# Performance work log

Measured on AMD Instinct MI355X. Metric: run time of the kernel, lower is better.

Reference implementation:

```python
import jax, jax.numpy as jnp
import numpy as np

CONF_T = 0.6   # default conf_threshold
IOU_T = 0.5    # default iou_threshold
ALPHA = 0.25
GAMMA = 2.0


def _nms_np(boxes, scores, iou_t):
    """Greedy NMS (torchvision semantics: keep while IoU <= iou_t), returns kept indices
    into `boxes`, sorted by decreasing score. Pure numpy; data-dependent output size."""
    order = np.argsort(-scores, kind="stable")
    b = boxes[order]
    x1, y1, x2, y2 = b[:, 0], b[:, 1], b[:, 2], b[:, 3]
    areas = (x2 - x1) * (y2 - y1)
    M = b.shape[0]
    suppressed = np.zeros(M, dtype=bool)
    keep = []
    for i in range(M):
        if suppressed[i]:
            continue
        keep.append(order[i])
        if i + 1 >= M:
            break
        xx1 = np.maximum(x1[i], x1[i + 1:]); yy1 = np.maximum(y1[i], y1[i + 1:])
        xx2 = np.minimum(x2[i], x2[i + 1:]); yy2 = np.minimum(y2[i], y2[i + 1:])
        inter = np.clip(xx2 - xx1, 0, None) * np.clip(yy2 - yy1, 0, None)
        iou = inter / (areas[i] + areas[i + 1:] - inter)
        suppressed[i + 1:] |= iou > iou_t
    return np.asarray(keep, dtype=np.int64)


def _select_indices(loc, conf):
    """Concrete (non-traced) confidence filtering + NMS; index selection is
    non-differentiable in the original torch code as well."""
    conf_np = np.asarray(conf)
    if conf_np.ndim == 3:
        conf_np = conf_np[0]                      # conf.squeeze(0)
    scores = conf_np.max(axis=1)                  # conf.max(dim=1)
    filt_idx = np.nonzero(scores > CONF_T)[0]     # mask filter
    boxes = np.asarray(loc)[0, filt_idx]          # loc[:, mask, :].squeeze(0)
    nms_score = conf_np[filt_idx, 0]              # score = filtered_conf[:, 0]
    nms_keep = _nms_np(boxes, nms_score, IOU_T)
    return filt_idx, nms_keep


def _smooth_l1_sum(pred, target):
    # SmoothL1Loss(beta=1.0, reduction='sum'); target (k,4) broadcasts against
    # pred (k,C,4) exactly as torch does (requires C == k).
    d = jnp.abs(pred - target)
    return jnp.sum(jnp.where(d < 1.0, 0.5 * d * d, d - 0.5))


def _loss(loc, conf, target_boxes, target_labels_f, filt_idx, nms_keep, k):
    conf2 = conf[0] if conf.ndim == 3 else conf   # (N,C)
    floc = loc[0, filt_idx]                       # (M,4) filtered boxes
    fconf = conf2[filt_idx]                       # (M,C)
    mloc = floc[nms_keep]                         # (P,4) NMS-kept boxes
    mconf = fconf[nms_keep]                       # (P,C)
    # torch.topk(matched_conf, k, dim=0): per-class column top-k
    vals, idx = jax.lax.top_k(mconf.T, k)         # (C,k) each
    vals, idx = vals.T, idx.T                     # (k,C)
    conf_bin = (vals[:, 0] > 0.5).astype(jnp.float32)   # (k,) hard 0/1 "logits"
    pred_box = mloc[idx]                          # (k,C,4) gather, as matched_loc[indices,:]
    loc_loss = _smooth_l1_sum(pred_box, target_boxes)
    # F.cross_entropy with 1-D input and float target => soft-label CE (scalar)
    ce = -jnp.sum(target_labels_f * jax.nn.log_softmax(conf_bin))
    p_t = jnp.exp(-ce)
    conf_loss = ALPHA * (1.0 - p_t) ** GAMMA * ce
    num_pos = jnp.asarray(nms_keep.shape[0], dtype=jnp.float32)
    return (loc_loss + conf_loss) / num_pos


def setup_inputs() -> dict:
    key = jax.random.key(0)
    k0, k1, k2, k3 = jax.random.split(key, 4)
    N, C, K = 8192, 20, 20
    return {
        "loc": jax.random.uniform(k0, (1, N, 4), dtype=jnp.float32),
        "conf": jax.random.uniform(k1, (1, N, C), dtype=jnp.float32),
        "target_boxes": jax.random.uniform(k2, (K, 4), dtype=jnp.float32),
        "target_labels": jax.random.randint(k3, (K,), 0, C).astype(jnp.int64),
    }


def reference(loc, conf, target_boxes, target_labels):
    filt_idx, nms_keep = _select_indices(loc, conf)
    if filt_idx.size == 0 or nms_keep.size == 0:
        return jnp.float32(0.001)
    k = int(target_labels.shape[0])
    return _loss(loc, conf, target_boxes,
                 target_labels.astype(jnp.float32),
                 jnp.asarray(filt_idx), jnp.asarray(nms_keep), k)
```

## Files before the change

kernel.cpp:

```cpp
#include <hip/hip_runtime.h>
#include <stdint.h>
#include <stddef.h>


#define NCAP 8192
#define WROW (NCAP / 64)

typedef unsigned long long u64;

constexpr size_t OFF_CNT   = 0;
constexpr size_t OFF_KEYS  = 256;
constexpr size_t OFF_SX1   = OFF_KEYS + 8ull * NCAP;
constexpr size_t OFF_SY1   = OFF_SX1 + 4ull * NCAP;
constexpr size_t OFF_SX2   = OFF_SY1 + 4ull * NCAP;
constexpr size_t OFF_SY2   = OFF_SX2 + 4ull * NCAP;
constexpr size_t OFF_AREA  = OFF_SY2 + 4ull * NCAP;
constexpr size_t OFF_SORIG = OFF_AREA + 4ull * NCAP;
constexpr size_t OFF_KEEPS = OFF_SORIG + 4ull * NCAP;
constexpr size_t OFF_KORIG = OFF_KEEPS + 4ull * NCAP;
constexpr size_t OFF_TOPV  = OFF_KORIG + 4ull * NCAP;
constexpr size_t OFF_TOPI  = OFF_TOPV + 4096;
constexpr size_t OFF_DIAG2 = OFF_TOPI + 4096;
constexpr size_t OFF_MASK  = OFF_DIAG2 + 16ull * NCAP;
constexpr size_t WS_NEED_MASK = OFF_MASK + 8ull * NCAP * WROW;

__device__ __forceinline__ void barrier_nodrain() {
  asm volatile("s_waitcnt lgkmcnt(0)" ::: "memory");
  __builtin_amdgcn_s_barrier();
  asm volatile("" ::: "memory");
}

template <int CTRL, int RMASK>
__device__ __forceinline__ unsigned or_dpp_step(unsigned x) {
  return x | (unsigned)__builtin_amdgcn_update_dpp(0, (int)x, CTRL, RMASK, 0xf, true);
}
__device__ __forceinline__ u64 wave_or64(u64 x) {
  unsigned lo = (unsigned)x, hi = (unsigned)(x >> 32);
  lo = or_dpp_step<0x111, 0xf>(lo); hi = or_dpp_step<0x111, 0xf>(hi);
  lo = or_dpp_step<0x112, 0xf>(lo); hi = or_dpp_step<0x112, 0xf>(hi);
  lo = or_dpp_step<0x114, 0xf>(lo); hi = or_dpp_step<0x114, 0xf>(hi);
  lo = or_dpp_step<0x118, 0xf>(lo); hi = or_dpp_step<0x118, 0xf>(hi);
  lo = or_dpp_step<0x142, 0xa>(lo); hi = or_dpp_step<0x142, 0xa>(hi);
  lo = or_dpp_step<0x143, 0xc>(lo); hi = or_dpp_step<0x143, 0xc>(hi);
  lo = (unsigned)__builtin_amdgcn_readlane((int)lo, 63);
  hi = (unsigned)__builtin_amdgcn_readlane((int)hi, 63);
  return ((u64)hi << 32) | lo;
}

#define SS1(M)                                                              \
  { int tt = base + (M) * 64 + l;                                           \
    u64 a = e[M];                                                           \
    unsigned slo = __shfl_xor((unsigned)a, (int)jj);                        \
    unsigned shi = __shfl_xor((unsigned)(a >> 32), (int)jj);                \
    u64 b = ((u64)shi << 32) | slo;                                         \
    bool up = ((tt & bk) == 0);                                             \
    bool lowr = ((l & (int)jj) == 0);                                       \
    bool tmin = (up == lowr);                                               \
    bool agtb = (a > b);                                                    \
    e[M] = (tmin == agtb) ? b : a; }

#define SSTEP() { SS1(0) SS1(1) SS1(2) SS1(3) SS1(4) SS1(5) SS1(6) SS1(7) }

#define CSW(A, B)                                                           \
  { int tt = base + (A) * 64 + l;                                           \
    bool up = ((tt & bk) == 0);                                             \
    u64 xa = e[A], xb = e[B];                                               \
    bool sw = up ? (xa > xb) : (xa < xb);                                   \
    e[A] = sw ? xb : xa; e[B] = sw ? xa : xb; }

#define RSTEP4() { CSW(0,4) CSW(1,5) CSW(2,6) CSW(3,7) }
#define RSTEP2() { CSW(0,2) CSW(1,3) CSW(4,6) CSW(5,7) }
#define RSTEP1() { CSW(0,1) CSW(2,3) CSW(4,5) CSW(6,7) }

__global__ __launch_bounds__(64) void k_psort(
    const float* __restrict__ conf, int N, int C,
    u64* __restrict__ keys) {
  const int l = threadIdx.x;
  const int base = blockIdx.x * 512;
  u64 e[8];
#pragma unroll
  for (int m = 0; m < 8; ++m) {
    int row = base + m * 64 + l;
    u64 key;
    if (row < N) {
      const float* cr = conf + (size_t)row * C;
      float mx = cr[0];
      for (int c = 1; c < C; ++c) mx = fmaxf(mx, cr[c]);
      unsigned int k32;
      if (mx > 0.6f) {
        union { float f; unsigned int u; } s; s.f = cr[0];
        unsigned int u = s.u;
        u = (u & 0x80000000u) ? ~u : (u | 0x80000000u);
        k32 = ~u;
        if (k32 == 0xFFFFFFFFu) k32 = 0xFFFFFFFEu;
      } else {
        k32 = 0xFFFFFFFFu;
      }
      key = ((u64)k32 << 32) | (unsigned int)row;
    } else {
      key = ((u64)0xFFFFFFFFu << 32);
    }
    e[m] = key;
  }
  for (unsigned bk = 2; bk <= 512; bk <<= 1) {
    unsigned j = bk >> 1;
    if (j == 256) { RSTEP4(); j = 128; }
    if (j == 128) { RSTEP2(); j = 64; }
    if (j == 64)  { RSTEP1(); j = 32; }
    for (unsigned jj = j; jj >= 1; jj >>= 1) SSTEP();
  }
#pragma unroll
  for (int m = 0; m < 8; ++m) keys[base + m * 64 + l] = e[m];
}

__global__ __launch_bounds__(1024) void k_merge(
    const float* __restrict__ loc,
    u64* __restrict__ keys, unsigned int* __restrict__ cnt,
    float* __restrict__ sx1, float* __restrict__ sy1,
    float* __restrict__ sx2, float* __restrict__ sy2,
    float* __restrict__ sarea, unsigned int* __restrict__ sorig) {
  __shared__ u64 sk[NCAP];
  __shared__ int wsum[16];
  const int tid = threadIdx.x;
  const int w = tid >> 6, l = tid & 63;
  const int base = w * 512;
  u64 e[8];
#pragma unroll
  for (int m = 0; m < 8; ++m) e[m] = keys[base + m * 64 + l];

  for (unsigned bk = 1024; bk <= NCAP; bk <<= 1) {
    unsigned j = bk >> 1;
    {
#pragma unroll
      for (int m = 0; m < 8; ++m) sk[base + m * 64 + l] = e[m];
      __syncthreads();
      for (unsigned j2 = bk >> 1; j2 >= 512; j2 >>= 1) {
        for (int tl = tid; tl < NCAP; tl += 1024) {
          unsigned p = (unsigned)tl ^ j2;
          if (p > (unsigned)tl) {
            bool up = ((tl & bk) == 0);
            u64 x = sk[tl], y = sk[p];
            bool sw = up ? (x > y) : (x < y);
            if (sw) { sk[tl] = y; sk[p] = x; }
          }
        }
        __syncthreads();
      }
#pragma unroll
      for (int m = 0; m < 8; ++m) e[m] = sk[base + m * 64 + l];
      __syncthreads();
      j = 256;
    }
    if (j == 256) { RSTEP4(); j = 128; }
    if (j == 128) { RSTEP2(); j = 64; }
    if (j == 64)  { RSTEP1(); j = 32; }
    for (unsigned jj = j; jj >= 1; jj >>= 1) SSTEP();
  }

  int cv = 0;
#pragma unroll
  for (int m = 0; m < 8; ++m) {
    int idx = base + m * 64 + l;
    u64 key = e[m];
    if ((key >> 32) != 0xFFFFFFFFull) ++cv;
    unsigned row = (unsigned)(key & 0xFFFFFFFFull);
    const float* b = loc + (size_t)row * 4;
    float x1 = b[0], y1 = b[1], x2 = b[2], y2 = b[3];
    sx1[idx] = x1; sy1[idx] = y1; sx2[idx] = x2; sy2[idx] = y2;
    sarea[idx] = (x2 - x1) * (y2 - y1);
    sorig[idx] = row;
  }
  for (int off = 32; off; off >>= 1) cv += __shfl_down(cv, off);
  if (l == 0) wsum[w] = cv;
  __syncthreads();
  if (tid == 0) {
    int s = 0;
    for (int i = 0; i < 16; ++i) s += wsum[i];
    cnt[0] = (unsigned int)s;
  }
}

__global__ __launch_bounds__(64) void k_mask(
    const float* __restrict__ sx1, const float* __restrict__ sy1,
    const float* __restrict__ sx2, const float* __restrict__ sy2,
    const float* __restrict__ sarea,
    u64* __restrict__ mask, u64* __restrict__ diagI) {
  if (blockIdx.y < (blockIdx.x & ~1u)) return;
  __shared__ float jx1[64], jy1[64], jx2[64], jy2[64], ja[64];
  int t = threadIdx.x;
  int jbase = blockIdx.y * 64;
  jx1[t] = sx1[jbase + t]; jy1[t] = sy1[jbase + t];
  jx2[t] = sx2[jbase + t]; jy2[t] = sy2[jbase + t];
  ja[t]  = sarea[jbase + t];
  __syncthreads();
  int i = blockIdx.x * 64 + t;
  float xi1 = sx1[i], yi1 = sy1[i], xi2 = sx2[i], yi2 = sy2[i], ai = sarea[i];
  u64 bits = 0ULL;
#pragma unroll 8
  for (int jj = 0; jj < 64; ++jj) {
    float xx1 = fmaxf(xi1, jx1[jj]);
    float yy1 = fmaxf(yi1, jy1[jj]);
    float xx2 = fminf(xi2, jx2[jj]);
    float yy2 = fminf(yi2, jy2[jj]);
    float w = fmaxf(xx2 - xx1, 0.0f);
    float h = fmaxf(yy2 - yy1, 0.0f);
    float inter = w * h;
    float den = ai + ja[jj] - inter;
    float iou = inter / den;
    if (iou > 0.5f) bits |= (1ULL << jj);
  }
  mask[(size_t)i * WROW + blockIdx.y] = bits;
  if ((blockIdx.y >> 1) == (blockIdx.x >> 1))
    diagI[((size_t)i << 1) + (blockIdx.y & 1)] = bits;
}

__global__ __launch_bounds__(1024) void k_scan(
    const u64* __restrict__ mask,
    const u64* __restrict__ diagIg,
    unsigned int* __restrict__ cnt,
    unsigned int* __restrict__ keeps) {
  __shared__ __align__(16) u64 ldsDiag[2 * NCAP];
  __shared__ __align__(16) u64 rem[WROW];
  __shared__ u64 ldsKA, ldsKB;
  __shared__ int ldsKb;
  const int tid = threadIdx.x;
  const int F = (int)cnt[0];
  const int nch = (F + 127) >> 7;
  const ulonglong2* __restrict__ m2 = (const ulonglong2*)mask;

  for (int i = tid; i < 2 * NCAP; i += 1024) ldsDiag[i] = diagIg[i];
  for (int w = tid; w < WROW; w += 1024) rem[w] = 0;

  const int p0 = tid & 63;
  const int g0 = tid >> 6;
  int K = 0;
  __syncthreads();

  for (int H = 0; H < nch; ++H) {
    const size_t gb = (size_t)H * 8192;
    const int base = H << 7;
    const bool ld = (p0 > H);
    ulonglong2 v0 = {0,0}, v1 = {0,0}, v2 = {0,0}, v3 = {0,0},
               v4 = {0,0}, v5 = {0,0}, v6 = {0,0}, v7 = {0,0};
    if (ld) {
      v0 = m2[gb + tid];
      v1 = m2[gb + tid + 1024];
      v2 = m2[gb + tid + 2048];
      v3 = m2[gb + tid + 3072];
      v4 = m2[gb + tid + 4096];
      v5 = m2[gb + tid + 5120];
      v6 = m2[gb + tid + 6144];
      v7 = m2[gb + tid + 7168];
    }
    barrier_nodrain();

    if (tid < 64) {
      ulonglong2 dAB = *(const ulonglong2*)&ldsDiag[(size_t)(base + tid) << 1];
      u64 DA = dAB.x, AB = dAB.y;
      u64 DB = ldsDiag[(((size_t)(base + 64 + tid)) << 1) + 1];
      ulonglong2 supP = *(const ulonglong2*)&rem[2 * H];
      u64 sup0 = supP.x, supB0 = supP.y;

      int remrows = F - base;
      u64 validA = (remrows >= 64) ? ~0ull : ((1ull << remrows) - 1ull);
      int r2 = remrows - 64;
      u64 validB = (r2 >= 64) ? ~0ull : ((r2 <= 0) ? 0ull : ((1ull << r2) - 1ull));

      u64 DfwdA = (tid < 63) ? (DA & (~0ull << (tid + 1))) : 0ull;
      u64 undec = validA & ~sup0;
      u64 dmask = ((undec >> tid) & 1ull) ? DfwdA : 0ull;
      u64 vuln = wave_or64(dmask);
      u64 dang = __ballot(dmask != 0ull);
      u64 involved = (dang | vuln) & undec;
      u64 keepA = undec & ~involved;
      u64 und2 = involved;
      {
        unsigned Flo = (unsigned)DfwdA, Fhi = (unsigned)(DfwdA >> 32);
        while (und2) {
          int rr = __builtin_ctzll(und2);
          keepA |= 1ull << rr;
          unsigned dlo = __builtin_amdgcn_readlane(Flo, rr);
          unsigned dhi = __builtin_amdgcn_readlane(Fhi, rr);
          und2 &= ~((((u64)dhi << 32) | (u64)dlo) | (1ull << rr));
        }
      }

      u64 abm = ((keepA >> tid) & 1ull) ? AB : 0ull;
      u64 supB = supB0 | wave_or64(abm);
      u64 DfwdB = (tid < 63) ? (DB & (~0ull << (tid + 1))) : 0ull;
      u64 undecB = validB & ~supB;
      u64 dmaskB = ((undecB >> tid) & 1ull) ? DfwdB : 0ull;
      u64 vulnB = wave_or64(dmaskB);
      u64 dangB = __ballot(dmaskB != 0ull);
      u64 involvedB = (dangB | vulnB) & undecB;
      u64 keepB = undecB & ~involvedB;
      u64 und2B = involvedB;
      {
        unsigned Flo = (unsigned)DfwdB, Fhi = (unsigned)(DfwdB >> 32);
        while (und2B) {
          int rr = __builtin_ctzll(und2B);
          keepB |= 1ull << rr;
          unsigned dlo = __builtin_amdgcn_readlane(Flo, rr);
          unsigned dhi = __builtin_amdgcn_readlane(Fhi, rr);
          und2B &= ~((((u64)dhi << 32) | (u64)dlo) | (1ull << rr));
        }
      }

      if (tid == 0) { ldsKA = keepA; ldsKB = keepB; ldsKb = K; }
      K += __popcll(keepA) + __popcll(keepB);
    }
    barrier_nodrain();

    const u64 keepA = ldsKA, keepB = ldsKB;

    if (g0 == 1) {
      const int l = p0;
      const int Kb = ldsKb;
      int pcA = __popcll(keepA);
      unsigned kloA = (unsigned)keepA, khiA = (unsigned)(keepA >> 32);
      int preA = __builtin_amdgcn_mbcnt_hi(khiA, __builtin_amdgcn_mbcnt_lo(kloA, 0));
      if ((keepA >> l) & 1ull) keeps[Kb + preA] = (unsigned)(base + l);
      unsigned kloB = (unsigned)keepB, khiB = (unsigned)(keepB >> 32);
      int preB = __builtin_amdgcn_mbcnt_hi(khiB, __builtin_amdgcn_mbcnt_lo(kloB, 0));
      if ((keepB >> l) & 1ull) keeps[Kb + pcA + preB] = (unsigned)(base + 64 + l);
    }

    if (ld && (keepA | keepB)) {
      u64 ax = 0, ay = 0;
      if ((keepA >> g0) & 1ull)        { ax |= v0.x; ay |= v0.y; }
      if ((keepA >> (g0+16)) & 1ull)   { ax |= v1.x; ay |= v1.y; }
      if ((keepA >> (g0+32)) & 1ull)   { ax |= v2.x; ay |= v2.y; }
      if ((keepA >> (g0+48)) & 1ull)   { ax |= v3.x; ay |= v3.y; }
      if ((keepB >> g0) & 1ull)        { ax |= v4.x; ay |= v4.y; }
      if ((keepB >> (g0+16)) & 1ull)   { ax |= v5.x; ay |= v5.y; }
      if ((keepB >> (g0+32)) & 1ull)   { ax |= v6.x; ay |= v6.y; }
      if ((keepB >> (g0+48)) & 1ull)   { ax |= v7.x; ay |= v7.y; }
      const int w0 = 2 * p0;
      if (ax) atomicOr(&rem[w0], ax);
      if (ay) atomicOr(&rem[w0 + 1], ay);
    }
  }
  if (tid == 0) cnt[1] = (unsigned int)K;
}

__global__ __launch_bounds__(256) void k_scan_nomask(
    const float* __restrict__ sx1, const float* __restrict__ sy1,
    const float* __restrict__ sx2, const float* __restrict__ sy2,
    const float* __restrict__ sarea,
    unsigned int* __restrict__ cnt,
    unsigned int* __restrict__ keeps) {
  __shared__ unsigned char sup[NCAP];
  __shared__ int sK;
  int tid = threadIdx.x;
  int F = (int)cnt[0];
  for (int j = tid; j < NCAP; j += 256) sup[j] = 0;
  if (tid == 0) sK = 0;
  __syncthreads();
  for (int i = 0; i < F; ++i) {
    if (!sup[i]) {
      if (tid == 0) keeps[sK++] = (unsigned int)i;
      float xi1 = sx1[i], yi1 = sy1[i], xi2 = sx2[i], yi2 = sy2[i], ai = sarea[i];
      for (int j = i + 1 + tid; j < F; j += 256) {
        if (sup[j]) continue;
        float xx1 = fmaxf(xi1, sx1[j]);
        float yy1 = fmaxf(yi1, sy1[j]);
        float xx2 = fminf(xi2, sx2[j]);
        float yy2 = fminf(yi2, sy2[j]);
        float w = fmaxf(xx2 - xx1, 0.0f);
        float h = fmaxf(yy2 - yy1, 0.0f);
        float inter = w * h;
        float iou = inter / (ai + sarea[j] - inter);
        if (iou > 0.5f) sup[j] = 1;
      }
    }
    __syncthreads();
  }
  if (tid == 0) cnt[1] = (unsigned int)sK;
}

__global__ __launch_bounds__(1024) void k_topk(
    const float* __restrict__ conf,
    const unsigned int* __restrict__ sorig,
    const unsigned int* __restrict__ keeps,
    const unsigned int* __restrict__ cnt,
    int C, int KT,
    float* __restrict__ topv, int* __restrict__ topi) {
  __shared__ float wlv[16];
  __shared__ int wli[16];
  __shared__ float ldsWv;
  __shared__ int ldsWj;
  const int tid = threadIdx.x;
  const int lane = tid & 63;
  const int wv_ = tid >> 6;
  const int c = blockIdx.x;
  const int M = (int)cnt[1];

  const float NEG = -3.402823466e+38f;
  float v[8];
#pragma unroll
  for (int k = 0; k < 8; ++k) {
    int j = tid + (k << 10);
    v[k] = (j < M) ? conf[(size_t)sorig[keeps[j]] * C + c] : NEG;
  }
  float bv = NEG; int bk_ = -1;
#pragma unroll
  for (int k = 0; k < 8; ++k)
    if (v[k] > bv) { bv = v[k]; bk_ = k; }
  int bj = (bk_ >= 0) ? (tid + (bk_ << 10)) : 0x7FFFFFFF;
  if (bv == NEG) bj = 0x7FFFFFFF;

  for (int t = 0; t < KT; ++t) {
    float rv = bv; int rj = bj;
#pragma unroll
    for (int off = 32; off; off >>= 1) {
      float v2 = __shfl_down(rv, off);
      int   j2 = __shfl_down(rj, off);
      if (v2 > rv || (v2 == rv && j2 < rj)) { rv = v2; rj = j2; }
    }
    if (lane == 0) { wlv[wv_] = rv; wli[wv_] = rj; }
    __syncthreads();
    if (wv_ == 0) {
      float fv = (lane < 16) ? wlv[lane] : NEG;
      int   fj = (lane < 16) ? wli[lane] : 0x7FFFFFFF;
#pragma unroll
      for (int off = 32; off; off >>= 1) {
        float v2 = __shfl_down(fv, off);
        int   j2 = __shfl_down(fj, off);
        if (v2 > fv || (v2 == fv && j2 < fj)) { fv = v2; fj = j2; }
      }
      if (lane == 0) {
        ldsWv = fv; ldsWj = fj;
        topv[c * KT + t] = fv;
        topi[c * KT + t] = (fj == 0x7FFFFFFF) ? 0 : fj;
      }
    }
    __syncthreads();
    const int wj = ldsWj;
    if (wj != 0x7FFFFFFF && (wj & 1023) == tid) {
      int kk = wj >> 10;
#pragma unroll
      for (int k = 0; k < 8; ++k)
        if (k == kk) v[k] = NEG;
      bv = NEG; bk_ = -1;
#pragma unroll
      for (int k = 0; k < 8; ++k)
        if (v[k] > bv) { bv = v[k]; bk_ = k; }
      bj = (bk_ >= 0) ? (tid + (bk_ << 10)) : 0x7FFFFFFF;
      if (bv == NEG) bj = 0x7FFFFFFF;
    }
  }
}

__global__ __launch_bounds__(256) void k_loss(
    const float* __restrict__ loc, const float* __restrict__ tb,
    const int* __restrict__ labels,
    const unsigned int* __restrict__ sorig,
    const unsigned int* __restrict__ keeps,
    const float* __restrict__ topv, const int* __restrict__ topi,
    const unsigned int* __restrict__ cnt, int C, int KT,
    float* __restrict__ out) {
  __shared__ float red[256];
  int tid = threadIdx.x;
  int F = (int)cnt[0];
  int M = (int)cnt[1];
  if (F == 0 || M == 0) {
    if (tid == 0) out[0] = 0.001f;
    return;
  }
  int total = KT * C * 4;
  float part = 0.0f;
  for (int e = tid; e < total; e += 256) {
    int d = e & 3;
    int q = e >> 2;
    int c = q % C;
    int i = q / C;
    int j = topi[c * KT + i];
    unsigned int orow = sorig[keeps[j]];
    float pred = loc[(size_t)orow * 4 + d];
    float tg = tb[c * 4 + d];
    float dd = fabsf(pred - tg);
    part += (dd < 1.0f) ? (0.5f * dd * dd) : (dd - 0.5f);
  }
  red[tid] = part;
  __syncthreads();
  for (int s = 128; s > 0; s >>= 1) {
    if (tid < s) red[tid] += red[tid + s];
    __syncthreads();
  }
  if (tid == 0) {
    float loc_loss = red[0];
    float mx = -3.402823466e+38f;
    for (int i = 0; i < KT; ++i) {
      float x = (topv[i] > 0.5f) ? 1.0f : 0.0f;
      mx = fmaxf(mx, x);
    }
    float ssum = 0.0f;
    for (int i = 0; i < KT; ++i) {
      float x = (topv[i] > 0.5f) ? 1.0f : 0.0f;
      ssum += expf(x - mx);
    }
    float lse = mx + logf(ssum);
    float ce = 0.0f;
    for (int i = 0; i < KT; ++i) {
      float x = (topv[i] > 0.5f) ? 1.0f : 0.0f;
      ce += (float)labels[i] * (x - lse);
    }
    ce = -ce;
    float pt = expf(-ce);
    float om = 1.0f - pt;
    float conf_loss = 0.25f * om * om * ce;
    out[0] = (loc_loss + conf_loss) / (float)M;
  }
}


extern "C" void kernel_launch(void* const* d_in, const int* in_sizes, int n_in,
                              void* d_out, int out_size, void* d_ws, size_t ws_size,
                              hipStream_t stream) {
  (void)n_in; (void)out_size;
  const float* loc    = (const float*)d_in[0];
  const float* conf   = (const float*)d_in[1];
  const float* tb     = (const float*)d_in[2];
  const int*   labels = (const int*)d_in[3];
  float* out = (float*)d_out;

  int N = in_sizes[0] / 4;
  if (N > NCAP) N = NCAP;
  int C  = (N > 0) ? (in_sizes[1] / N) : 20;
  int KT = in_sizes[3];

  char* ws = (char*)d_ws;
  unsigned int* cnt   = (unsigned int*)(ws + OFF_CNT);
  u64*          keys  = (u64*)(ws + OFF_KEYS);
  float*        sx1   = (float*)(ws + OFF_SX1);
  float*        sy1   = (float*)(ws + OFF_SY1);
  float*        sx2   = (float*)(ws + OFF_SX2);
  float*        sy2   = (float*)(ws + OFF_SY2);
  float*        sarea = (float*)(ws + OFF_AREA);
  unsigned int* sorig = (unsigned int*)(ws + OFF_SORIG);
  unsigned int* keeps = (unsigned int*)(ws + OFF_KEEPS);
  float*        topv  = (float*)(ws + OFF_TOPV);
  int*          topi  = (int*)(ws + OFF_TOPI);
  u64*          diagI = (u64*)(ws + OFF_DIAG2);
  u64*          mask  = (u64*)(ws + OFF_MASK);

  bool use_mask = (ws_size >= WS_NEED_MASK);

  k_psort<<<16, 64, 0, stream>>>(conf, N, C, keys);
  k_merge<<<1, 1024, 0, stream>>>(loc, keys, cnt,
                                  sx1, sy1, sx2, sy2, sarea, sorig);
  if (use_mask) {
    k_mask<<<dim3(WROW, WROW), 64, 0, stream>>>(sx1, sy1, sx2, sy2, sarea,
                                                mask, diagI);
    k_scan<<<1, 1024, 0, stream>>>(mask, diagI, cnt, keeps);
  } else {
    k_scan_nomask<<<1, 256, 0, stream>>>(sx1, sy1, sx2, sy2, sarea, cnt, keeps);
  }
  k_topk<<<C, 1024, 0, stream>>>(conf, sorig, keeps, cnt, C, KT, topv, topi);
  k_loss<<<1, 256, 0, stream>>>(loc, tb, labels, sorig, keeps, topv, topi, cnt, C, KT, out);
}
```

Before: 305.2 us.

## Skip loading all-zero mask tiles in NMS scan using per-tile nonzero bitmaps

The mask kernel now records, for each 64-row block and column-pair chunk, a ballot bitmap of which rows have any nonzero overlap bits, OR-ed atomically into a small summary array that k_psort zeroes first. The single-block scan kernel reads this summary (prefetching the next chunk's entry) and skips global loads of mask words whose rows are known to be zero. This targets the serial scan's memory traffic, which matters because sparse IoU masks are mostly zero. It costs extra atomics in k_mask and a larger workspace, and it only takes effect when the workspace is big enough.

```diff
diff --git a/kernel.cpp b/kernel.cpp
--- a/kernel.cpp
+++ b/kernel.cpp
@@ -5,6 +5,7 @@
 
 #define NCAP 8192
 #define WROW (NCAP / 64)
+#define NBX  (NCAP / 64)
 
 typedef unsigned long long u64;
 
@@ -23,6 +24,8 @@
 constexpr size_t OFF_DIAG2 = OFF_TOPI + 4096;
 constexpr size_t OFF_MASK  = OFF_DIAG2 + 16ull * NCAP;
 constexpr size_t WS_NEED_MASK = OFF_MASK + 8ull * NCAP * WROW;
+constexpr size_t OFF_CNZ   = WS_NEED_MASK;
+constexpr size_t WS_NEED_NZ = OFF_CNZ + 8ull * 64 * NBX;
 
 __device__ __forceinline__ void barrier_nodrain() {
   asm volatile("s_waitcnt lgkmcnt(0)" ::: "memory");
@@ -74,9 +77,14 @@
 
 __global__ __launch_bounds__(64) void k_psort(
     const float* __restrict__ conf, int N, int C,
-    u64* __restrict__ keys) {
+    u64* __restrict__ keys, u64* __restrict__ colnz) {
   const int l = threadIdx.x;
   const int base = blockIdx.x * 512;
+  if (colnz) {
+    size_t b = (size_t)(blockIdx.x * 64 + l) * 8;
+#pragma unroll
+    for (int i = 0; i < 8; ++i) colnz[b + i] = 0ull;
+  }
   u64 e[8];
 #pragma unroll
   for (int m = 0; m < 8; ++m) {
@@ -184,7 +192,8 @@
     const float* __restrict__ sx1, const float* __restrict__ sy1,
     const float* __restrict__ sx2, const float* __restrict__ sy2,
     const float* __restrict__ sarea,
-    u64* __restrict__ mask, u64* __restrict__ diagI) {
+    u64* __restrict__ mask, u64* __restrict__ diagI,
+    u64* __restrict__ cnz) {
   if (blockIdx.y < (blockIdx.x & ~1u)) return;
   __shared__ float jx1[64], jy1[64], jx2[64], jy2[64], ja[64];
   int t = threadIdx.x;
@@ -212,11 +221,18 @@
   mask[(size_t)i * WROW + blockIdx.y] = bits;
   if ((blockIdx.y >> 1) == (blockIdx.x >> 1))
     diagI[((size_t)i << 1) + (blockIdx.y & 1)] = bits;
-}
-
+  if (cnz != nullptr) {
+    u64 nzb = __ballot(bits != 0ULL);
+    if (t == 0 && nzb)
+      atomicOr((unsigned long long*)&cnz[((size_t)(blockIdx.y >> 1)) * NBX + blockIdx.x], nzb);
+  }
+}
+
+template <int USE_NZ>
 __global__ __launch_bounds__(1024) void k_scan(
     const u64* __restrict__ mask,
     const u64* __restrict__ diagIg,
+    const u64* __restrict__ cnzv,
     unsigned int* __restrict__ cnt,
     unsigned int* __restrict__ keeps) {
   __shared__ __align__(16) u64 ldsDiag[2 * NCAP];
@@ -234,24 +250,33 @@
   const int p0 = tid & 63;
   const int g0 = tid >> 6;
   int K = 0;
+
+  const ulonglong2* __restrict__ cz =
+      (const ulonglong2*)cnzv + (size_t)p0 * (NBX / 2);
+  ulonglong2 nzp = {0, 0};
+  if (USE_NZ && nch > 0) nzp = cz[0];
   __syncthreads();
 
   for (int H = 0; H < nch; ++H) {
     const size_t gb = (size_t)H * 8192;
     const int base = H << 7;
     const bool ld = (p0 > H);
+    u64 nzA = ~0ull, nzB = ~0ull;
+    if (USE_NZ) { nzA = nzp.x; nzB = nzp.y; }
     ulonglong2 v0 = {0,0}, v1 = {0,0}, v2 = {0,0}, v3 = {0,0},
                v4 = {0,0}, v5 = {0,0}, v6 = {0,0}, v7 = {0,0};
     if (ld) {
-      v0 = m2[gb + tid];
-      v1 = m2[gb + tid + 1024];
-      v2 = m2[gb + tid + 2048];
-      v3 = m2[gb + tid + 3072];
-      v4 = m2[gb + tid + 4096];
-      v5 = m2[gb + tid + 5120];
-      v6 = m2[gb + tid + 6144];
-      v7 = m2[gb + tid + 7168];
-    }
+      if ((nzA >> (g0 +  0)) & 1ull) v0 = m2[gb + tid];
+      if ((nzA >> (g0 + 16)) & 1ull) v1 = m2[gb + tid + 1024];
+      if ((nzA >> (g0 + 32)) & 1ull) v2 = m2[gb + tid + 2048];
+      if ((nzA >> (g0 + 48)) & 1ull) v3 = m2[gb + tid + 3072];
+      if ((nzB >> (g0 +  0)) & 1ull) v4 = m2[gb + tid + 4096];
+      if ((nzB >> (g0 + 16)) & 1ull) v5 = m2[gb + tid + 5120];
+      if ((nzB >> (g0 + 32)) & 1ull) v6 = m2[gb + tid + 6144];
+      if ((nzB >> (g0 + 48)) & 1ull) v7 = m2[gb + tid + 7168];
+    }
+    ulonglong2 nzn = {0, 0};
+    if (USE_NZ && H + 1 < nch) nzn = cz[H + 1];
     barrier_nodrain();
 
     if (tid < 64) {
@@ -339,6 +364,7 @@
       if (ax) atomicOr(&rem[w0], ax);
       if (ay) atomicOr(&rem[w0 + 1], ay);
     }
+    nzp = nzn;
   }
   if (tid == 0) cnt[1] = (unsigned int)K;
 }
@@ -543,16 +569,22 @@
   int*          topi  = (int*)(ws + OFF_TOPI);
   u64*          diagI = (u64*)(ws + OFF_DIAG2);
   u64*          mask  = (u64*)(ws + OFF_MASK);
+  u64*          colnz = (u64*)(ws + OFF_CNZ);
 
   bool use_mask = (ws_size >= WS_NEED_MASK);
-
-  k_psort<<<16, 64, 0, stream>>>(conf, N, C, keys);
+  bool use_nz   = (ws_size >= WS_NEED_NZ);
+
+  k_psort<<<16, 64, 0, stream>>>(conf, N, C, keys, use_nz ? colnz : nullptr);
   k_merge<<<1, 1024, 0, stream>>>(loc, keys, cnt,
                                   sx1, sy1, sx2, sy2, sarea, sorig);
   if (use_mask) {
     k_mask<<<dim3(WROW, WROW), 64, 0, stream>>>(sx1, sy1, sx2, sy2, sarea,
-                                                mask, diagI);
-    k_scan<<<1, 1024, 0, stream>>>(mask, diagI, cnt, keeps);
+                                                mask, diagI,
+                                                use_nz ? colnz : nullptr);
+    if (use_nz)
+      k_scan<1><<<1, 1024, 0, stream>>>(mask, diagI, colnz, cnt, keeps);
+    else
+      k_scan<0><<<1, 1024, 0, stream>>>(mask, diagI, colnz, cnt, keeps);
   } else {
     k_scan_nomask<<<1, 256, 0, stream>>>(sx1, sy1, sx2, sy2, sarea, cnt, keeps);
   }
```

New measurement: 318.8 us. 1.04x slower.
